# Optimization experiments

Hardware: AMD Instinct MI355X
Metric: run time of the kernel (lower is better)

## Reference

```python
import jax, jax.numpy as jnp
import numpy as np

EMBEDDING_DIM = 256
NUM_EMBEDDINGS = 8192
COMMITMENT_COST = 0.25
DECAY = 0.99
EPSILON = 1e-5


def setup_inputs() -> dict:
    key = jax.random.key(0)
    k1, k2 = jax.random.split(key)
    inputs = jax.random.normal(k1, (16, 32, 32, EMBEDDING_DIM), dtype=jnp.float32)
    # VarianceScaling(distribution='uniform'), fan_in scaling over [D, K]
    limit = float(np.sqrt(3.0 / EMBEDDING_DIM))
    embeddings = jax.random.uniform(k2, (EMBEDDING_DIM, NUM_EMBEDDINGS),
                                    minval=-limit, maxval=limit, dtype=jnp.float32)
    return {
        'inputs': inputs,
        'embeddings': embeddings,
        'ema_cs_hidden': jnp.zeros((NUM_EMBEDDINGS,), jnp.float32),
        'ema_dw_hidden': embeddings,  # hk initializes ema_dw to the embeddings
        'counter': 0,
        'is_training': 1,
    }


def reference(inputs, embeddings, ema_cs_hidden, ema_dw_hidden, counter, is_training):
    flat = inputs.reshape(-1, EMBEDDING_DIM)                        # [N, D]
    distances = (jnp.sum(flat ** 2, axis=1, keepdims=True)
                 - 2.0 * (flat @ embeddings)
                 + jnp.sum(embeddings ** 2, axis=0, keepdims=True))  # [N, K]
    encoding_indices = jnp.argmax(-distances, axis=1)                # [N]
    encodings = jax.nn.one_hot(encoding_indices, NUM_EMBEDDINGS,
                               dtype=distances.dtype)                # [N, K]
    idx = encoding_indices.reshape(inputs.shape[:-1])
    quantized = embeddings.T[idx]                                    # gather codebook
    e_latent_loss = jnp.mean((jax.lax.stop_gradient(quantized) - inputs) ** 2)
    loss = COMMITMENT_COST * e_latent_loss

    if is_training:
        # haiku ExponentialMovingAverage with zero-debias
        new_counter = counter + 1
        debias = 1.0 - DECAY ** new_counter
        cs_hidden = ema_cs_hidden * DECAY + jnp.sum(encodings, axis=0) * (1.0 - DECAY)
        cs_avg = cs_hidden / debias                                  # [K]
        dw = flat.T @ encodings                                      # [D, K] scatter-add as GEMM
        dw_hidden = ema_dw_hidden * DECAY + dw * (1.0 - DECAY)
        dw_avg = dw_hidden / debias
        n = jnp.sum(cs_avg)
        cs_norm = (cs_avg + EPSILON) / (n + NUM_EMBEDDINGS * EPSILON) * n
        new_embeddings = dw_avg / cs_norm[None, :]                   # [D, K]
    else:
        new_embeddings = embeddings

    # straight-through estimator
    quantized_st = inputs + jax.lax.stop_gradient(quantized - inputs)
    avg_probs = jnp.mean(encodings, axis=0)
    perplexity = jnp.exp(-jnp.sum(avg_probs * jnp.log(avg_probs + 1e-10)))
    return (quantized_st, loss, perplexity, idx, new_embeddings)
```

## Files before the change

kernel.cpp:

```cpp
#include <hip/hip_runtime.h>
#include <math.h>

#define DD 256
#define KK 8192
#define NN 16384
#define DECAYF 0.99f
#define EPSF 1e-5f
#define TAU 4e-3f

#define O_Q    0
#define O_LOSS 4194304
#define O_PERP 4194305
#define O_IDX  4194306
#define O_EMB  4210690

typedef float f32x4 __attribute__((ext_vector_type(4)));
typedef _Float16 f16x8 __attribute__((ext_vector_type(8)));

__device__ __forceinline__ unsigned short f2h(float f) {
  union { _Float16 h; unsigned short u; } c;
  c.h = (_Float16)f;
  return c.u;
}

__device__ __forceinline__ void gll16(const void* g, void* l) {
  __builtin_amdgcn_global_load_lds((const __attribute__((address_space(1))) void*)g,
                                   (__attribute__((address_space(3))) void*)l, 16, 0, 0);
}

#define DPPI(x, ctrl) __builtin_amdgcn_update_dpp((x), (x), (ctrl), 0xf, 0xf, true)
#define DPPF(x, ctrl) __int_as_float(__builtin_amdgcn_update_dpp(__float_as_int(x), __float_as_int(x), (ctrl), 0xf, 0xf, true))

__global__ void k_convert_xe(const float* __restrict__ x, unsigned short* __restrict__ Ah,
                             const float* __restrict__ emb, unsigned short* __restrict__ Eh,
                             float* __restrict__ embT, float* __restrict__ esq,
                             unsigned long long* __restrict__ keys) {
  __shared__ float ld[32 * 33];
  int bx = blockIdx.x;
  int t = threadIdx.x;
  if (bx < 4096) {
    int i = bx * 256 + t;
    float4 v = ((const float4*)x)[i];
    ushort4 h;
    h.x = f2h(v.x); h.y = f2h(v.y); h.z = f2h(v.z); h.w = f2h(v.w);
    ((ushort4*)Ah)[i] = h;
    return;
  }
  int eb = bx - 4096;
  if (eb < 64) keys[eb * 256 + t] = ~0ull;
  int k0 = (eb & 255) * 32, d0 = (eb >> 8) * 32;
  {
    int din = t >> 3, kq = (t & 7) * 4;
    float4 v = *(const float4*)(emb + (size_t)(d0 + din) * KK + k0 + kq);
    ld[din * 33 + kq + 0] = v.x; ld[din * 33 + kq + 1] = v.y;
    ld[din * 33 + kq + 2] = v.z; ld[din * 33 + kq + 3] = v.w;
  }
  __syncthreads();
  int kout = t >> 3, dq = (t & 7) * 4;
  float f0 = ld[(dq + 0) * 33 + kout], f1 = ld[(dq + 1) * 33 + kout];
  float f2 = ld[(dq + 2) * 33 + kout], f3 = ld[(dq + 3) * 33 + kout];
  size_t o = (size_t)(k0 + kout) * DD + d0 + dq;
  float4 fv; fv.x = f0; fv.y = f1; fv.z = f2; fv.w = f3;
  *(float4*)(embT + o) = fv;
  ushort4 hv;
  hv.x = f2h(f0); hv.y = f2h(f1); hv.z = f2h(f2); hv.w = f2h(f3);
  *(ushort4*)(Eh + o) = hv;
  float p = (f0 * f0 + f1 * f1) + (f2 * f2 + f3 * f3);
  p += __shfl_xor(p, 1, 64);
  p += __shfl_xor(p, 2, 64);
  p += __shfl_xor(p, 4, 64);
  if ((t & 7) == 0) atomicAdd(esq + k0 + kout, p);
}

__launch_bounds__(256, 2)
__global__ void k_dist_mfma(const unsigned short* __restrict__ Ah, const unsigned short* __restrict__ Bh,
                            const float* __restrict__ esq,
                            float* __restrict__ part1, float* __restrict__ part2,
                            int* __restrict__ partidx) {
  __shared__ __align__(16) unsigned short sB[8192];

  const int tid = threadIdx.x;
  const int w = tid >> 6, lane = tid & 63;
  const int kb = blockIdx.x, nb = blockIdx.y;
  const int row0 = nb * 128, col0 = kb * 128;
  const int m = lane & 15, q = lane >> 4;

  size_t gB[4];
  int lbB[4];
  #pragma unroll
  for (int s = 0; s < 4; ++s) {
    int g = w * 4 + s;
    int r = g * 8 + (lane >> 3);
    int c = (lane & 7) ^ (r & 7);
    gB[s] = (size_t)(col0 + r) * DD + c * 8;
    lbB[s] = g * 512;
  }

  const unsigned short* pA0 = Ah + (size_t)(row0 + w * 32 + m) * DD + q * 8;
  const unsigned short* pA1 = pA0 + 16 * DD;

  f32x4 acc[2][8];
  #pragma unroll
  for (int i = 0; i < 2; ++i)
    #pragma unroll
    for (int j = 0; j < 8; ++j) acc[i][j] = (f32x4)0.f;

  for (int it = 0; it < 4; ++it) {
    const int d0 = it * 64;
    __syncthreads();
    #pragma unroll
    for (int s = 0; s < 4; ++s) gll16(Bh + gB[s] + d0, sB + lbB[s]);
    f16x8 a[2][2];
    #pragma unroll
    for (int kk = 0; kk < 2; ++kk) {
      a[kk][0] = *(const f16x8*)(pA0 + d0 + kk * 32);
      a[kk][1] = *(const f16x8*)(pA1 + d0 + kk * 32);
    }
    __syncthreads();
    #pragma unroll
    for (int kk = 0; kk < 2; ++kk) {
      #pragma unroll
      for (int j = 0; j < 8; ++j) {
        int cn = j * 16 + m;
        int slot = (kk * 4 + q) ^ (cn & 7);
        f16x8 b = *(const f16x8*)(sB + cn * 64 + slot * 8);
        acc[0][j] = __builtin_amdgcn_mfma_f32_16x16x32_f16(a[kk][0], b, acc[0][j], 0, 0, 0);
        acc[1][j] = __builtin_amdgcn_mfma_f32_16x16x32_f16(a[kk][1], b, acc[1][j], 0, 0, 0);
      }
    }
  }

  float eq[8];
  #pragma unroll
  for (int j = 0; j < 8; ++j) eq[j] = esq[col0 + j * 16 + m];

  #define RSTAGE(CTRL) {                                  \
    float ov = DPPF(m1, CTRL);                            \
    int   oi = DPPI(bi, CTRL);                            \
    float o2 = DPPF(m2, CTRL);                            \
    m2 = fminf(fminf(m2, o2), fmaxf(m1, ov));             \
    bool p = ov < m1;                                     \
    m1 = fminf(m1, ov);                                   \
    bi = p ? oi : bi;                                     \
  }
  #pragma unroll
  for (int i = 0; i < 2; ++i) {
    #pragma unroll
    for (int reg = 0; reg < 4; ++reg) {
      float m1 = 3.402823466e+38f, m2 = 3.402823466e+38f;
      int bi = 0;
      #pragma unroll
      for (int j = 0; j < 8; ++j) {
        float dd = fmaf(-2.0f, acc[i][j][reg], eq[j]);
        bool p = dd < m1;
        m2 = fminf(m2, fmaxf(dd, m1));
        m1 = fminf(m1, dd);
        bi = p ? (col0 + j * 16 + m) : bi;
      }
      RSTAGE(0xB1)
      RSTAGE(0x4E)
      RSTAGE(0x141)
      RSTAGE(0x140)
      if (m == 0) {
        int prow = row0 + w * 32 + i * 16 + q * 4 + reg;
        int pidx = prow * 64 + kb;
        part1[pidx] = m1; part2[pidx] = m2; partidx[pidx] = bi;
      }
    }
  }
  #undef RSTAGE
}

__global__ void k_argmin2(float* __restrict__ part1, float* __restrict__ part2,
                          const int* __restrict__ partidx, int* __restrict__ idxw,
                          int* __restrict__ listc, int* __restrict__ list) {
  int w = threadIdx.x >> 6, l = threadIdx.x & 63;
  int row = blockIdx.x * 4 + w;
  int f = blockIdx.x * 256 + threadIdx.x;
  float m1 = part1[f], m2 = part2[f];
  int bi = partidx[f];
  part1[f] = 0.f;
  part2[f] = 0.f;
  #pragma unroll
  for (int st = 1; st < 64; st <<= 1) {
    float ov = __shfl_xor(m1, st, 64);
    int   oi = __shfl_xor(bi, st, 64);
    float o2 = __shfl_xor(m2, st, 64);
    m2 = fminf(fminf(m2, o2), fmaxf(m1, ov));
    bool p = ov < m1;
    m1 = fminf(m1, ov);
    bi = p ? oi : bi;
  }
  if (l == 0) {
    idxw[row] = bi;
    if (m2 - m1 < TAU) { int pos = atomicAdd(listc, 1); list[pos] = row; }
  }
}

__global__ void k_rescore(const float* __restrict__ x, const float* __restrict__ emb,
                          const int* __restrict__ listc, const int* __restrict__ list,
                          unsigned long long* __restrict__ keys) {
  __shared__ float se[8192];
  __shared__ double red[256];
  const int t = threadIdx.x;
  const int k0 = blockIdx.x * 32;
  int cnt = *listc;
  if ((int)blockIdx.y >= cnt) return;
  #pragma unroll
  for (int i = 0; i < 32; ++i) {
    int elem = i * 256 + t;
    int d = elem >> 5, c = elem & 31;
    se[d * 32 + c] = emb[(size_t)d * KK + k0 + c];
  }
  __syncthreads();
  const int c = t & 31, p = t >> 5;
  for (int li = blockIdx.y; li < cnt; li += gridDim.y) {
    int row = list[li];
    const float* xr = x + (size_t)row * DD;
    double acc = 0.0;
    #pragma unroll
    for (int j = 0; j < 32; ++j) {
      int d = p * 32 + j;
      double df = (double)xr[d] - (double)se[d * 32 + c];
      acc = fma(df, df, acc);
    }
    red[c * 8 + p] = acc;
    __syncthreads();
    if (t < 64) {
      unsigned long long key = ~0ull;
      if (t < 32) {
        double dist = 0.0;
        #pragma unroll
        for (int qq = 0; qq < 8; ++qq) dist += red[t * 8 + qq];
        key = ((unsigned long long)__double_as_longlong(dist) & ~0x1FFFull)
              | (unsigned long long)(k0 + t);
      }
      #pragma unroll
      for (int s = 1; s < 64; s <<= 1) {
        unsigned long long o = __shfl_xor(key, s, 64);
        if (o < key) key = o;
      }
      if (t == 0) atomicMin(&keys[row], key);
    }
    __syncthreads();
  }
}

__global__ void k_gather(const float* __restrict__ x, const float* __restrict__ embT,
                         const int* __restrict__ idxw, const unsigned long long* __restrict__ keys,
                         const int* __restrict__ train,
                         float* __restrict__ outq, float* __restrict__ outidx,
                         float* __restrict__ dwT, float* __restrict__ counts,
                         float* __restrict__ loss_part) {
  int w = threadIdx.x >> 6, l = threadIdx.x & 63;
  int n = blockIdx.x * 4 + w;
  unsigned long long kv = keys[n];
  int k = (kv != ~0ull) ? (int)(kv & 0x1FFFull) : idxw[n];
  float4 xv = ((const float4*)(x + (size_t)n * DD))[l];
  float4 qv = ((const float4*)(embT + (size_t)k * DD))[l];
  int d = l * 4;

  ((float4*)(outq + (size_t)n * DD))[l] = qv;

  float e0 = qv.x - xv.x, e1 = qv.y - xv.y, e2 = qv.z - xv.z, e3 = qv.w - xv.w;
  float ls = (e0 * e0 + e1 * e1) + (e2 * e2 + e3 * e3);

  if (*train) {
    const float wdw = 1.0f - DECAYF;
    float* base = dwT + (size_t)k * DD + d;
    atomicAdd(base + 0, xv.x * wdw);
    atomicAdd(base + 1, xv.y * wdw);
    atomicAdd(base + 2, xv.z * wdw);
    atomicAdd(base + 3, xv.w * wdw);
  }

  #pragma unroll
  for (int s = 1; s < 64; s <<= 1) ls += __shfl_xor(ls, s, 64);
  if (l == 0) {
    atomicAdd(&loss_part[blockIdx.x & 255], ls);
    atomicAdd(&counts[k], 1.0f);
    outidx[n] = (float)k;
  }
}

__global__ void k_stats(const float* __restrict__ counts, const float* __restrict__ ema_cs,
                        const int* __restrict__ counter, const int* __restrict__ train,
                        const float* __restrict__ loss_part, float* __restrict__ csn,
                        float* __restrict__ outloss, float* __restrict__ outperp) {
  __shared__ float s_n[4], s_e[4], s_l[4], s_tot[1];
  int tid = threadIdx.x;
  float debias = 1.0f - powf(DECAYF, (float)(*counter + 1));
  float nloc = 0.f, eloc = 0.f;
  float lloc = loss_part[tid];
  float avg[32];
  for (int i = 0; i < 32; ++i) {
    int k = tid + i * 256;
    float c = counts[k];
    float h = ema_cs[k] * DECAYF + c * (1.0f - DECAYF);
    float a = h / debias;
    avg[i] = a;
    nloc += a;
    float p = c * (1.0f / 16384.0f);
    eloc += p * logf(p + 1e-10f);
  }
  #pragma unroll
  for (int s = 1; s < 64; s <<= 1) {
    nloc += __shfl_xor(nloc, s, 64);
    eloc += __shfl_xor(eloc, s, 64);
    lloc += __shfl_xor(lloc, s, 64);
  }
  int w = tid >> 6, lane = tid & 63;
  if (lane == 0) { s_n[w] = nloc; s_e[w] = eloc; s_l[w] = lloc; }
  __syncthreads();
  if (tid == 0) {
    float nt = (s_n[0] + s_n[1]) + (s_n[2] + s_n[3]);
    float et = (s_e[0] + s_e[1]) + (s_e[2] + s_e[3]);
    float lt = (s_l[0] + s_l[1]) + (s_l[2] + s_l[3]);
    s_tot[0] = nt;
    outperp[0] = expf(-et);
    outloss[0] = 0.25f * (lt / 4194304.0f);
  }
  __syncthreads();
  float nsum = s_tot[0];
  float denom = nsum + 8192.0f * EPSF;
  for (int i = 0; i < 32; ++i) {
    int k = tid + i * 256;
    csn[k] = (avg[i] + EPSF) / denom * nsum;
  }
}

__global__ void k_final(const float* __restrict__ dwT, const float* __restrict__ ema_dw,
                        const float* __restrict__ emb, const float* __restrict__ csn,
                        const int* __restrict__ counter, const int* __restrict__ train,
                        float* __restrict__ out4) {
  __shared__ float ld[32 * 33];
  int t = threadIdx.x;
  int k0 = blockIdx.x * 32, d0 = blockIdx.y * 32;
  if (*train) {
    {
      int ki = t >> 3, dq = (t & 7) * 4;
      float4 v = *(const float4*)(dwT + (size_t)(k0 + ki) * DD + d0 + dq);
      ld[ki * 33 + dq + 0] = v.x; ld[ki * 33 + dq + 1] = v.y;
      ld[ki * 33 + dq + 2] = v.z; ld[ki * 33 + dq + 3] = v.w;
    }
    __syncthreads();
    int dout = t >> 3, kq = (t & 7) * 4;
    size_t o = (size_t)(d0 + dout) * KK + k0 + kq;
    float4 e = *(const float4*)(ema_dw + o);
    float4 c = *(const float4*)(csn + k0 + kq);
    float inv = 1.0f / (1.0f - powf(DECAYF, (float)(*counter + 1)));
    float4 r;
    r.x = fmaf(e.x, DECAYF, ld[(kq + 0) * 33 + dout]) * inv / c.x;
    r.y = fmaf(e.y, DECAYF, ld[(kq + 1) * 33 + dout]) * inv / c.y;
    r.z = fmaf(e.z, DECAYF, ld[(kq + 2) * 33 + dout]) * inv / c.z;
    r.w = fmaf(e.w, DECAYF, ld[(kq + 3) * 33 + dout]) * inv / c.w;
    *(float4*)(out4 + o) = r;
  } else {
    int dout = t >> 3, kq = (t & 7) * 4;
    size_t o = (size_t)(d0 + dout) * KK + k0 + kq;
    *(float4*)(out4 + o) = *(const float4*)(emb + o);
  }
}

extern "C" void kernel_launch(void* const* d_in, const int* in_sizes, int n_in,
                              void* d_out, int out_size, void* d_ws, size_t ws_size,
                              hipStream_t stream) {
  (void)in_sizes; (void)n_in; (void)out_size; (void)ws_size;
  const float* x      = (const float*)d_in[0];
  const float* emb    = (const float*)d_in[1];
  const float* ema_cs = (const float*)d_in[2];
  const float* ema_dw = (const float*)d_in[3];
  const int*   counter = (const int*)d_in[4];
  const int*   train   = (const int*)d_in[5];

  float* out = (float*)d_out;
  float* outq    = out + O_Q;
  float* outloss = out + O_LOSS;
  float* outperp = out + O_PERP;
  float* outidx  = out + O_IDX;
  float* out4    = out + O_EMB;

  char* W = (char*)d_ws;
  unsigned short* Ah   = (unsigned short*)(W);
  unsigned short* Eh   = (unsigned short*)(W + 8388608);
  float* embT          = (float*)(W + 12582912);
  float* part1         = (float*)(W + 20971520);
  float* part2         = (float*)(W + 25165824);
  int*   partidx       = (int*)(W + 29360128);
  float* dwT           = part1;
  unsigned long long* keys = (unsigned long long*)(W + 33554432);
  float* esq           = (float*)(W + 33685504);
  float* csn           = (float*)(W + 33718272);
  float* counts        = (float*)(W + 33751040);
  float* loss_part     = (float*)(W + 33783808);
  int*   listc         = (int*)(W + 33784832);
  int*   list          = (int*)(W + 33784836);
  int*   idxw          = (int*)(W + 33850372);

  hipMemsetAsync(esq, 0, 99332, stream);

  k_convert_xe<<<6144, 256, 0, stream>>>(x, Ah, emb, Eh, embT, esq, keys);
  k_dist_mfma<<<dim3(64, 128), 256, 0, stream>>>(Ah, Eh, esq, part1, part2, partidx);
  k_argmin2<<<4096, 256, 0, stream>>>(part1, part2, partidx, idxw, listc, list);
  k_rescore<<<dim3(256, 8), 256, 0, stream>>>(x, emb, listc, list, keys);
  k_gather<<<4096, 256, 0, stream>>>(x, embT, idxw, keys, train, outq, outidx, dwT, counts, loss_part);
  k_stats<<<1, 256, 0, stream>>>(counts, ema_cs, counter, train, loss_part, csn, outloss, outperp);
  k_final<<<dim3(256, 8), 256, 0, stream>>>(dwT, ema_dw, emb, csn, counter, train, out4);
}
```

Measured before the change: 363.0 us.

## Fold argmin reduction into GEMM epilogue via atomic keys and fuse stats kernel

The distance GEMM epilogue now packs each partial best and second-best distance into order-preserving 64-bit keys and reduces them with atomicMin directly into per-row keys. This removes the partial-result buffers and the separate argmin kernel. The rescore kernel builds its own per-block list of ambiguous rows from the keys. The stats kernel is folded into the final kernel, with each block recomputing the count normalisation. The esq atomics are replaced by per-slice partial writes, and workspace zeroing moves into the convert kernel, dropping the memset. The trade-off is global atomic contention in the GEMM epilogue and redundant count reductions across all final blocks.

```diff
diff --git a/kernel.cpp b/kernel.cpp
--- a/kernel.cpp
+++ b/kernel.cpp
@@ -28,13 +28,22 @@
                                    (__attribute__((address_space(3))) void*)l, 16, 0, 0);
 }
 
+__device__ __forceinline__ unsigned sortenc(float f) {
+  unsigned u = __float_as_uint(f);
+  return (u >> 31) ? ~u : (u | 0x80000000u);
+}
+__device__ __forceinline__ float sortdec(unsigned u) {
+  return (u & 0x80000000u) ? __uint_as_float(u ^ 0x80000000u) : __uint_as_float(~u);
+}
+
 #define DPPI(x, ctrl) __builtin_amdgcn_update_dpp((x), (x), (ctrl), 0xf, 0xf, true)
 #define DPPF(x, ctrl) __int_as_float(__builtin_amdgcn_update_dpp(__float_as_int(x), __float_as_int(x), (ctrl), 0xf, 0xf, true))
 
 __global__ void k_convert_xe(const float* __restrict__ x, unsigned short* __restrict__ Ah,
                              const float* __restrict__ emb, unsigned short* __restrict__ Eh,
-                             float* __restrict__ embT, float* __restrict__ esq,
-                             unsigned long long* __restrict__ keys) {
+                             float* __restrict__ embT, float* __restrict__ esqp,
+                             float* __restrict__ dwT, unsigned long long* __restrict__ keysAll,
+                             float* __restrict__ counts, float* __restrict__ loss_part) {
   __shared__ float ld[32 * 33];
   int bx = blockIdx.x;
   int t = threadIdx.x;
@@ -44,14 +53,22 @@
     ushort4 h;
     h.x = f2h(v.x); h.y = f2h(v.y); h.z = f2h(v.z); h.w = f2h(v.w);
     ((ushort4*)Ah)[i] = h;
+    if (t < 128) ((float4*)dwT)[bx * 128 + t] = make_float4(0.f, 0.f, 0.f, 0.f);
+    if (bx < 96) {
+      keysAll[bx * 512 + t] = ~0ull;
+      keysAll[bx * 512 + 256 + t] = ~0ull;
+    } else if (bx < 128) {
+      counts[(bx - 96) * 256 + t] = 0.f;
+    } else if (bx == 128) {
+      loss_part[t] = 0.f;
+    }
     return;
   }
   int eb = bx - 4096;
-  if (eb < 64) keys[eb * 256 + t] = ~0ull;
-  int k0 = (eb & 255) * 32, d0 = (eb >> 8) * 32;
+  int k0 = (eb & 255) * 32, d0b = eb >> 8;
   {
     int din = t >> 3, kq = (t & 7) * 4;
-    float4 v = *(const float4*)(emb + (size_t)(d0 + din) * KK + k0 + kq);
+    float4 v = *(const float4*)(emb + (size_t)(d0b * 32 + din) * KK + k0 + kq);
     ld[din * 33 + kq + 0] = v.x; ld[din * 33 + kq + 1] = v.y;
     ld[din * 33 + kq + 2] = v.z; ld[din * 33 + kq + 3] = v.w;
   }
@@ -59,7 +76,7 @@
   int kout = t >> 3, dq = (t & 7) * 4;
   float f0 = ld[(dq + 0) * 33 + kout], f1 = ld[(dq + 1) * 33 + kout];
   float f2 = ld[(dq + 2) * 33 + kout], f3 = ld[(dq + 3) * 33 + kout];
-  size_t o = (size_t)(k0 + kout) * DD + d0 + dq;
+  size_t o = (size_t)(k0 + kout) * DD + d0b * 32 + dq;
   float4 fv; fv.x = f0; fv.y = f1; fv.z = f2; fv.w = f3;
   *(float4*)(embT + o) = fv;
   ushort4 hv;
@@ -69,14 +86,14 @@
   p += __shfl_xor(p, 1, 64);
   p += __shfl_xor(p, 2, 64);
   p += __shfl_xor(p, 4, 64);
-  if ((t & 7) == 0) atomicAdd(esq + k0 + kout, p);
+  if ((t & 7) == 0) esqp[(size_t)(k0 + kout) * 8 + d0b] = p;
 }
 
 __launch_bounds__(256, 2)
 __global__ void k_dist_mfma(const unsigned short* __restrict__ Ah, const unsigned short* __restrict__ Bh,
-                            const float* __restrict__ esq,
-                            float* __restrict__ part1, float* __restrict__ part2,
-                            int* __restrict__ partidx) {
+                            const float* __restrict__ esqp,
+                            unsigned long long* __restrict__ key1,
+                            unsigned long long* __restrict__ key2) {
   __shared__ __align__(16) unsigned short sB[8192];
 
   const int tid = threadIdx.x;
@@ -132,7 +149,12 @@
 
   float eq[8];
   #pragma unroll
-  for (int j = 0; j < 8; ++j) eq[j] = esq[col0 + j * 16 + m];
+  for (int j = 0; j < 8; ++j) {
+    int cn = col0 + j * 16 + m;
+    const float4* ep = (const float4*)esqp + cn * 2;
+    float4 sa = ep[0], sb = ep[1];
+    eq[j] = ((sa.x + sa.y) + (sa.z + sa.w)) + ((sb.x + sb.y) + (sb.z + sb.w));
+  }
 
   #define RSTAGE(CTRL) {                                  \
     float ov = DPPF(m1, CTRL);                            \
@@ -163,49 +185,43 @@
       RSTAGE(0x140)
       if (m == 0) {
         int prow = row0 + w * 32 + i * 16 + q * 4 + reg;
-        int pidx = prow * 64 + kb;
-        part1[pidx] = m1; part2[pidx] = m2; partidx[pidx] = bi;
+        unsigned long long k1 = ((unsigned long long)sortenc(m1) << 32) | (unsigned)bi;
+        unsigned long long k2 = ((unsigned long long)sortenc(m2) << 32) | 0xFFFFFFFFull;
+        unsigned long long old = atomicMin(&key1[prow], k1);
+        unsigned long long cand = old > k1 ? old : k1;
+        atomicMin(&key2[prow], cand < k2 ? cand : k2);
       }
     }
   }
   #undef RSTAGE
 }
 
-__global__ void k_argmin2(float* __restrict__ part1, float* __restrict__ part2,
-                          const int* __restrict__ partidx, int* __restrict__ idxw,
-                          int* __restrict__ listc, int* __restrict__ list) {
-  int w = threadIdx.x >> 6, l = threadIdx.x & 63;
-  int row = blockIdx.x * 4 + w;
-  int f = blockIdx.x * 256 + threadIdx.x;
-  float m1 = part1[f], m2 = part2[f];
-  int bi = partidx[f];
-  part1[f] = 0.f;
-  part2[f] = 0.f;
-  #pragma unroll
-  for (int st = 1; st < 64; st <<= 1) {
-    float ov = __shfl_xor(m1, st, 64);
-    int   oi = __shfl_xor(bi, st, 64);
-    float o2 = __shfl_xor(m2, st, 64);
-    m2 = fminf(fminf(m2, o2), fmaxf(m1, ov));
-    bool p = ov < m1;
-    m1 = fminf(m1, ov);
-    bi = p ? oi : bi;
-  }
-  if (l == 0) {
-    idxw[row] = bi;
-    if (m2 - m1 < TAU) { int pos = atomicAdd(listc, 1); list[pos] = row; }
-  }
-}
-
 __global__ void k_rescore(const float* __restrict__ x, const float* __restrict__ emb,
-                          const int* __restrict__ listc, const int* __restrict__ list,
-                          unsigned long long* __restrict__ keys) {
+                          const unsigned long long* __restrict__ key1,
+                          const unsigned long long* __restrict__ key2,
+                          unsigned long long* __restrict__ keysR) {
   __shared__ float se[8192];
   __shared__ double red[256];
+  __shared__ int lcnt;
+  __shared__ unsigned short lrows[2048];
   const int t = threadIdx.x;
+  if (t == 0) lcnt = 0;
+  __syncthreads();
+  const int base = blockIdx.y * 2048;
+  #pragma unroll
+  for (int i = 0; i < 8; ++i) {
+    int r = base + i * 256 + t;
+    float m1f = sortdec((unsigned)(key1[r] >> 32));
+    float m2f = sortdec((unsigned)(key2[r] >> 32));
+    if (m2f - m1f < TAU) {
+      int pos = atomicAdd(&lcnt, 1);
+      lrows[pos] = (unsigned short)(i * 256 + t);
+    }
+  }
+  __syncthreads();
+  const int cnt = lcnt;
+  if (cnt == 0) return;
   const int k0 = blockIdx.x * 32;
-  int cnt = *listc;
-  if ((int)blockIdx.y >= cnt) return;
   #pragma unroll
   for (int i = 0; i < 32; ++i) {
     int elem = i * 256 + t;
@@ -214,8 +230,8 @@
   }
   __syncthreads();
   const int c = t & 31, p = t >> 5;
-  for (int li = blockIdx.y; li < cnt; li += gridDim.y) {
-    int row = list[li];
+  for (int li = 0; li < cnt; ++li) {
+    int row = base + lrows[li];
     const float* xr = x + (size_t)row * DD;
     double acc = 0.0;
     #pragma unroll
@@ -240,22 +256,23 @@
         unsigned long long o = __shfl_xor(key, s, 64);
         if (o < key) key = o;
       }
-      if (t == 0) atomicMin(&keys[row], key);
+      if (t == 0) atomicMin(&keysR[row], key);
     }
     __syncthreads();
   }
 }
 
 __global__ void k_gather(const float* __restrict__ x, const float* __restrict__ embT,
-                         const int* __restrict__ idxw, const unsigned long long* __restrict__ keys,
+                         const unsigned long long* __restrict__ key1,
+                         const unsigned long long* __restrict__ keysR,
                          const int* __restrict__ train,
                          float* __restrict__ outq, float* __restrict__ outidx,
                          float* __restrict__ dwT, float* __restrict__ counts,
                          float* __restrict__ loss_part) {
   int w = threadIdx.x >> 6, l = threadIdx.x & 63;
   int n = blockIdx.x * 4 + w;
-  unsigned long long kv = keys[n];
-  int k = (kv != ~0ull) ? (int)(kv & 0x1FFFull) : idxw[n];
+  unsigned long long kv = keysR[n];
+  int k = (kv != ~0ull) ? (int)(kv & 0x1FFFull) : (int)(key1[n] & 0x1FFFull);
   float4 xv = ((const float4*)(x + (size_t)n * DD))[l];
   float4 qv = ((const float4*)(embT + (size_t)k * DD))[l];
   int d = l * 4;
@@ -283,60 +300,58 @@
   }
 }
 
-__global__ void k_stats(const float* __restrict__ counts, const float* __restrict__ ema_cs,
+__global__ void k_final(const float* __restrict__ dwT, const float* __restrict__ ema_dw,
+                        const float* __restrict__ emb, const float* __restrict__ counts,
+                        const float* __restrict__ ema_cs, const float* __restrict__ loss_part,
                         const int* __restrict__ counter, const int* __restrict__ train,
-                        const float* __restrict__ loss_part, float* __restrict__ csn,
-                        float* __restrict__ outloss, float* __restrict__ outperp) {
-  __shared__ float s_n[4], s_e[4], s_l[4], s_tot[1];
-  int tid = threadIdx.x;
-  float debias = 1.0f - powf(DECAYF, (float)(*counter + 1));
-  float nloc = 0.f, eloc = 0.f;
-  float lloc = loss_part[tid];
-  float avg[32];
-  for (int i = 0; i < 32; ++i) {
-    int k = tid + i * 256;
-    float c = counts[k];
-    float h = ema_cs[k] * DECAYF + c * (1.0f - DECAYF);
-    float a = h / debias;
-    avg[i] = a;
-    nloc += a;
-    float p = c * (1.0f / 16384.0f);
-    eloc += p * logf(p + 1e-10f);
-  }
-  #pragma unroll
-  for (int s = 1; s < 64; s <<= 1) {
-    nloc += __shfl_xor(nloc, s, 64);
-    eloc += __shfl_xor(eloc, s, 64);
-    lloc += __shfl_xor(lloc, s, 64);
-  }
-  int w = tid >> 6, lane = tid & 63;
-  if (lane == 0) { s_n[w] = nloc; s_e[w] = eloc; s_l[w] = lloc; }
-  __syncthreads();
-  if (tid == 0) {
-    float nt = (s_n[0] + s_n[1]) + (s_n[2] + s_n[3]);
-    float et = (s_e[0] + s_e[1]) + (s_e[2] + s_e[3]);
-    float lt = (s_l[0] + s_l[1]) + (s_l[2] + s_l[3]);
-    s_tot[0] = nt;
-    outperp[0] = expf(-et);
-    outloss[0] = 0.25f * (lt / 4194304.0f);
-  }
-  __syncthreads();
-  float nsum = s_tot[0];
-  float denom = nsum + 8192.0f * EPSF;
-  for (int i = 0; i < 32; ++i) {
-    int k = tid + i * 256;
-    csn[k] = (avg[i] + EPSF) / denom * nsum;
-  }
-}
-
-__global__ void k_final(const float* __restrict__ dwT, const float* __restrict__ ema_dw,
-                        const float* __restrict__ emb, const float* __restrict__ csn,
-                        const int* __restrict__ counter, const int* __restrict__ train,
-                        float* __restrict__ out4) {
+                        float* __restrict__ out4, float* __restrict__ outloss,
+                        float* __restrict__ outperp) {
   __shared__ float ld[32 * 33];
+  __shared__ float s_red[4], s_l[4], s_e[4];
+  __shared__ float csn_s[32];
   int t = threadIdx.x;
   int k0 = blockIdx.x * 32, d0 = blockIdx.y * 32;
+  int w = t >> 6, lane = t & 63;
+
+  if (blockIdx.x == 0 && blockIdx.y == 0) {
+    float lloc = loss_part[t];
+    float eloc = 0.f;
+    for (int i = 0; i < 32; ++i) {
+      float cc = counts[t + i * 256];
+      float pp = cc * (1.0f / 16384.0f);
+      eloc += pp * logf(pp + 1e-10f);
+    }
+    #pragma unroll
+    for (int s = 1; s < 64; s <<= 1) {
+      lloc += __shfl_xor(lloc, s, 64);
+      eloc += __shfl_xor(eloc, s, 64);
+    }
+    if (lane == 0) { s_l[w] = lloc; s_e[w] = eloc; }
+    __syncthreads();
+    if (t == 0) {
+      outloss[0] = 0.25f * (((s_l[0] + s_l[1]) + (s_l[2] + s_l[3])) / 4194304.0f);
+      outperp[0] = expf(-((s_e[0] + s_e[1]) + (s_e[2] + s_e[3])));
+    }
+  }
+
   if (*train) {
+    float debias = 1.0f - powf(DECAYF, (float)(*counter + 1));
+    float inv = 1.0f / debias;
+    float nloc = 0.f;
+    for (int i = 0; i < 32; ++i) {
+      int k = t + i * 256;
+      nloc += fmaf(counts[k], 1.0f - DECAYF, ema_cs[k] * DECAYF);
+    }
+    #pragma unroll
+    for (int s = 1; s < 64; s <<= 1) nloc += __shfl_xor(nloc, s, 64);
+    if (lane == 0) s_red[w] = nloc;
+    __syncthreads();
+    float nsum = ((s_red[0] + s_red[1]) + (s_red[2] + s_red[3])) * inv;
+    if (t < 32) {
+      int k = k0 + t;
+      float a = fmaf(counts[k], 1.0f - DECAYF, ema_cs[k] * DECAYF) * inv;
+      csn_s[t] = (a + EPSF) / (nsum + 8192.0f * EPSF) * nsum;
+    }
     {
       int ki = t >> 3, dq = (t & 7) * 4;
       float4 v = *(const float4*)(dwT + (size_t)(k0 + ki) * DD + d0 + dq);
@@ -347,13 +362,11 @@
     int dout = t >> 3, kq = (t & 7) * 4;
     size_t o = (size_t)(d0 + dout) * KK + k0 + kq;
     float4 e = *(const float4*)(ema_dw + o);
-    float4 c = *(const float4*)(csn + k0 + kq);
-    float inv = 1.0f / (1.0f - powf(DECAYF, (float)(*counter + 1)));
     float4 r;
-    r.x = fmaf(e.x, DECAYF, ld[(kq + 0) * 33 + dout]) * inv / c.x;
-    r.y = fmaf(e.y, DECAYF, ld[(kq + 1) * 33 + dout]) * inv / c.y;
-    r.z = fmaf(e.z, DECAYF, ld[(kq + 2) * 33 + dout]) * inv / c.z;
-    r.w = fmaf(e.w, DECAYF, ld[(kq + 3) * 33 + dout]) * inv / c.w;
+    r.x = fmaf(e.x, DECAYF, ld[(kq + 0) * 33 + dout]) * inv / csn_s[kq + 0];
+    r.y = fmaf(e.y, DECAYF, ld[(kq + 1) * 33 + dout]) * inv / csn_s[kq + 1];
+    r.z = fmaf(e.z, DECAYF, ld[(kq + 2) * 33 + dout]) * inv / csn_s[kq + 2];
+    r.w = fmaf(e.w, DECAYF, ld[(kq + 3) * 33 + dout]) * inv / csn_s[kq + 3];
     *(float4*)(out4 + o) = r;
   } else {
     int dout = t >> 3, kq = (t & 7) * 4;
@@ -384,26 +397,17 @@
   unsigned short* Ah   = (unsigned short*)(W);
   unsigned short* Eh   = (unsigned short*)(W + 8388608);
   float* embT          = (float*)(W + 12582912);
-  float* part1         = (float*)(W + 20971520);
-  float* part2         = (float*)(W + 25165824);
-  int*   partidx       = (int*)(W + 29360128);
-  float* dwT           = part1;
-  unsigned long long* keys = (unsigned long long*)(W + 33554432);
-  float* esq           = (float*)(W + 33685504);
-  float* csn           = (float*)(W + 33718272);
-  float* counts        = (float*)(W + 33751040);
-  float* loss_part     = (float*)(W + 33783808);
-  int*   listc         = (int*)(W + 33784832);
-  int*   list          = (int*)(W + 33784836);
-  int*   idxw          = (int*)(W + 33850372);
-
-  hipMemsetAsync(esq, 0, 99332, stream);
-
-  k_convert_xe<<<6144, 256, 0, stream>>>(x, Ah, emb, Eh, embT, esq, keys);
-  k_dist_mfma<<<dim3(64, 128), 256, 0, stream>>>(Ah, Eh, esq, part1, part2, partidx);
-  k_argmin2<<<4096, 256, 0, stream>>>(part1, part2, partidx, idxw, listc, list);
-  k_rescore<<<dim3(256, 8), 256, 0, stream>>>(x, emb, listc, list, keys);
-  k_gather<<<4096, 256, 0, stream>>>(x, embT, idxw, keys, train, outq, outidx, dwT, counts, loss_part);
-  k_stats<<<1, 256, 0, stream>>>(counts, ema_cs, counter, train, loss_part, csn, outloss, outperp);
-  k_final<<<dim3(256, 8), 256, 0, stream>>>(dwT, ema_dw, emb, csn, counter, train, out4);
-}
+  float* dwT           = (float*)(W + 20971520);
+  unsigned long long* key1  = (unsigned long long*)(W + 29360128);
+  unsigned long long* key2  = (unsigned long long*)(W + 29491200);
+  unsigned long long* keysR = (unsigned long long*)(W + 29622272);
+  float* esqp          = (float*)(W + 29753344);
+  float* counts        = (float*)(W + 30015488);
+  float* loss_part     = (float*)(W + 30048256);
+
+  k_convert_xe<<<6144, 256, 0, stream>>>(x, Ah, emb, Eh, embT, esqp, dwT, key1, counts, loss_part);
+  k_dist_mfma<<<dim3(64, 128), 256, 0, stream>>>(Ah, Eh, esqp, key1, key2);
+  k_rescore<<<dim3(256, 8), 256, 0, stream>>>(x, emb, key1, key2, keysR);
+  k_gather<<<4096, 256, 0, stream>>>(x, embT, key1, keysR, train, outq, outidx, dwT, counts, loss_part);
+  k_final<<<dim3(256, 8), 256, 0, stream>>>(dwT, ema_dw, emb, counts, ema_cs, loss_part, counter, train, out4, outloss, outperp);
+}
```

After: 468.8 us. 1.29x slower.
